# Kernel optimization log

Hardware: AMD Instinct MI355X
Metric: run time of the kernel (lower is better)

Reference implementation:

```python
import jax, jax.numpy as jnp
import numpy as np

N, E, D, H, G = 50000, 800000, 128, 128, 64
EPS = 1e-5


def setup_inputs() -> dict:
    key = jax.random.key(0)
    ks = jax.random.split(key, 16)
    x = jax.random.normal(ks[0], (N, D), dtype=jnp.float32)
    edge_index = jax.random.randint(ks[1], (2, E), 0, N, dtype=jnp.int64)
    batch = jnp.sort(jax.random.randint(ks[2], (N,), 0, G, dtype=jnp.int64))
    dims = [D, H, H, H]
    params = {}
    for i in range(3):
        params[f"W{i}"] = jax.random.normal(ks[3 + i], (dims[i], dims[i + 1]), dtype=jnp.float32) * (1.0 / np.sqrt(dims[i]).astype(np.float32))
        params[f"b{i}"] = jnp.zeros((dims[i + 1],), jnp.float32)
        params[f"g{i}"] = jnp.ones((dims[i + 1],), jnp.float32)   # BN gamma
        params[f"be{i}"] = jnp.zeros((dims[i + 1],), jnp.float32)  # BN beta
    params["Wout"] = jax.random.normal(ks[10], (H, 1), dtype=jnp.float32) * (1.0 / np.sqrt(H).astype(np.float32))
    params["bout"] = jnp.zeros((1,), jnp.float32)
    return {"x": x, "edge_index": edge_index, "batch": batch, **params}


def _gcn_forward(x, edge_index, batch, Ws, bs, gs, bes, Wout, bout):
    n = x.shape[0]
    loop = jnp.arange(n)
    # GCNConv default: add self-loops, symmetric degree normalization
    src = jnp.concatenate([edge_index[0], loop])
    dst = jnp.concatenate([edge_index[1], loop])
    deg = jax.ops.segment_sum(jnp.ones_like(dst, x.dtype), dst, num_segments=n)
    dinv = jax.lax.rsqrt(jnp.maximum(deg, 1.0))  # deg >= 1 from self-loops
    norm = dinv[src] * dinv[dst]                 # [E+N]
    h = x
    for W, b, g, be in zip(Ws, bs, gs, bes):
        h = h @ W                                               # transform [N,C]
        msg = h[src] * norm[:, None]                            # gather [E+N,C]
        h = jax.ops.segment_sum(msg, dst, num_segments=n) + b   # scatter-add
        # BatchNorm1d (training-mode batch statistics over nodes)
        mu = jnp.mean(h, axis=0)
        var = jnp.var(h, axis=0)
        h = (h - mu) * jax.lax.rsqrt(var + EPS) * g + be
        h = jax.nn.relu(h)
        # dropout: identity (deterministic eval reference)
    counts = jax.ops.segment_sum(jnp.ones((n,), h.dtype), batch, num_segments=G)
    pooled = jax.ops.segment_sum(h, batch, num_segments=G) / jnp.maximum(counts, 1.0)[:, None]
    return jax.nn.sigmoid(pooled @ Wout + bout)  # [G,1]


def reference(x, edge_index, batch, W0, b0, g0, be0, W1, b1, g1, be1, W2, b2, g2, be2, Wout, bout):
    return _gcn_forward(x, edge_index, batch,
                        (W0, W1, W2), (b0, b1, b2), (g0, g1, g2), (be0, be1, be2),
                        Wout, bout)
```

## Files before the change

### kernel.cpp

```cpp
#include <hip/hip_runtime.h>

#define EPSBN 1e-5f

using bf16x8 = __attribute__((ext_vector_type(8))) short;
using f32x4  = __attribute__((ext_vector_type(4))) float;

__device__ __forceinline__ unsigned short f2bf(float f) {
    unsigned u = __builtin_bit_cast(unsigned, f);
    unsigned r = (u + 0x7FFFu + ((u >> 16) & 1u)) >> 16;
    return (unsigned short)r;
}
__device__ __forceinline__ float bf2f(unsigned short s) {
    unsigned u = ((unsigned)s) << 16;
    return __builtin_bit_cast(float, u);
}


__global__ void k_deg(const int* __restrict__ dst, int E, int* __restrict__ deg) {
    int i = blockIdx.x * blockDim.x + threadIdx.x;
    if (i < E) atomicAdd(&deg[dst[i]], 1);
}

__global__ void k_dinv(const int* __restrict__ deg, int N, float* __restrict__ dinv) {
    int i = blockIdx.x * blockDim.x + threadIdx.x;
    if (i < N) dinv[i] = rsqrtf((float)(deg[i] + 1));
}

__global__ void k_scan1(const int* __restrict__ deg, int N, int* __restrict__ rs, int* __restrict__ blk) {
    __shared__ int sh[256];
    int tid = threadIdx.x;
    int i = blockIdx.x * 256 + tid;
    int v = (i < N) ? deg[i] : 0;
    sh[tid] = v; __syncthreads();
    for (int off = 1; off < 256; off <<= 1) {
        int t = (tid >= off) ? sh[tid - off] : 0;
        __syncthreads();
        sh[tid] += t;
        __syncthreads();
    }
    if (i < N) rs[i] = sh[tid] - v;
    if (tid == 255) blk[blockIdx.x] = sh[255];
}

__global__ void k_scan2(const int* __restrict__ blk, int nb, int* __restrict__ blkoff) {
    __shared__ int sh[1024];
    int tid = threadIdx.x;
    int v = (tid < nb) ? blk[tid] : 0;
    sh[tid] = v; __syncthreads();
    for (int off = 1; off < 1024; off <<= 1) {
        int t = (tid >= off) ? sh[tid - off] : 0;
        __syncthreads();
        sh[tid] += t;
        __syncthreads();
    }
    if (tid < nb) blkoff[tid] = sh[tid] - v;
}

__global__ void k_scan3(int* __restrict__ rs, int N, const int* __restrict__ blkoff) {
    int i = blockIdx.x * blockDim.x + threadIdx.x;
    if (i < N) rs[i] += blkoff[i >> 8];
}

__global__ void k_fill(const int* __restrict__ src, const int* __restrict__ dst, int E,
                       const int* __restrict__ rs, int* __restrict__ cursor, int* __restrict__ col) {
    int i = blockIdx.x * blockDim.x + threadIdx.x;
    if (i < E) {
        int d = dst[i];
        int pos = rs[d] + atomicAdd(&cursor[d], 1);
        col[pos] = src[i];
    }
}


__global__ __launch_bounds__(256) void k_gemm(const unsigned short* __restrict__ Abf,
                                              const float* __restrict__ Af,
                                              const float* __restrict__ W,
                                              unsigned short* __restrict__ C, int N,
                                              const float* __restrict__ scale,
                                              const float* __restrict__ shift, int mode) {
    __shared__ unsigned short Asw[128 * 128];
    __shared__ unsigned short Wt[128 * 128];
    int tid = threadIdx.x;
    int r0 = blockIdx.x * 128;

    {
        int n = tid & 127, kh = tid >> 7;
        const float* wp = &W[(kh * 64) * 128 + n];
        #pragma unroll
        for (int kb = 0; kb < 8; ++kb) {
            unsigned short t8[8];
            #pragma unroll
            for (int e = 0; e < 8; ++e)
                t8[e] = f2bf(wp[(kb * 8 + e) * 128]);
            int byte = (n * 256 + kh * 128 + kb * 16) ^ ((n & 7) << 4);
            *reinterpret_cast<uint4*>(reinterpret_cast<char*>(Wt) + byte) =
                *reinterpret_cast<const uint4*>(t8);
        }
    }
    if (mode == 0) {
        const float* ap = &Af[(size_t)r0 * 128];
        #pragma unroll
        for (int j = 0; j < 8; ++j) {
            int u = tid + j * 256;
            int row = u >> 4, cg = u & 15;
            unsigned short t8[8] = {0,0,0,0,0,0,0,0};
            if (r0 + row < N) {
                float4 a0 = *reinterpret_cast<const float4*>(ap + row * 128 + cg * 8);
                float4 a1 = *reinterpret_cast<const float4*>(ap + row * 128 + cg * 8 + 4);
                t8[0]=f2bf(a0.x); t8[1]=f2bf(a0.y); t8[2]=f2bf(a0.z); t8[3]=f2bf(a0.w);
                t8[4]=f2bf(a1.x); t8[5]=f2bf(a1.y); t8[6]=f2bf(a1.z); t8[7]=f2bf(a1.w);
            }
            int byte = (row * 256 + cg * 16) ^ ((row & 7) << 4);
            *reinterpret_cast<uint4*>(reinterpret_cast<char*>(Asw) + byte) =
                *reinterpret_cast<const uint4*>(t8);
        }
    } else {
        const unsigned short* ap = &Abf[(size_t)r0 * 128];
        #pragma unroll
        for (int j = 0; j < 8; ++j) {
            int u = tid + j * 256;
            int row = u >> 4, cg = u & 15;
            unsigned short t8[8] = {0,0,0,0,0,0,0,0};
            if (r0 + row < N) {
                ushort4 v0 = *reinterpret_cast<const ushort4*>(ap + (size_t)row * 128 + cg * 8);
                ushort4 v1 = *reinterpret_cast<const ushort4*>(ap + (size_t)row * 128 + cg * 8 + 4);
                float4 sc0 = *reinterpret_cast<const float4*>(&scale[cg * 8]);
                float4 sc1 = *reinterpret_cast<const float4*>(&scale[cg * 8 + 4]);
                float4 sf0 = *reinterpret_cast<const float4*>(&shift[cg * 8]);
                float4 sf1 = *reinterpret_cast<const float4*>(&shift[cg * 8 + 4]);
                t8[0] = f2bf(fmaxf(bf2f(v0.x) * sc0.x + sf0.x, 0.f));
                t8[1] = f2bf(fmaxf(bf2f(v0.y) * sc0.y + sf0.y, 0.f));
                t8[2] = f2bf(fmaxf(bf2f(v0.z) * sc0.z + sf0.z, 0.f));
                t8[3] = f2bf(fmaxf(bf2f(v0.w) * sc0.w + sf0.w, 0.f));
                t8[4] = f2bf(fmaxf(bf2f(v1.x) * sc1.x + sf1.x, 0.f));
                t8[5] = f2bf(fmaxf(bf2f(v1.y) * sc1.y + sf1.y, 0.f));
                t8[6] = f2bf(fmaxf(bf2f(v1.z) * sc1.z + sf1.z, 0.f));
                t8[7] = f2bf(fmaxf(bf2f(v1.w) * sc1.w + sf1.w, 0.f));
            }
            int byte = (row * 256 + cg * 16) ^ ((row & 7) << 4);
            *reinterpret_cast<uint4*>(reinterpret_cast<char*>(Asw) + byte) =
                *reinterpret_cast<const uint4*>(t8);
        }
    }
    __syncthreads();

    int wv = tid >> 6, lane = tid & 63;
    int lr = lane & 15, lk = lane >> 4;
    f32x4 acc[2][8] = {};
    #pragma unroll
    for (int kk = 0; kk < 4; ++kk) {
        bf16x8 af[2], bf[8];
        #pragma unroll
        for (int mf = 0; mf < 2; ++mf) {
            int ar = wv * 32 + mf * 16 + lr;
            int byte = (ar * 256 + kk * 64 + lk * 16) ^ ((ar & 7) << 4);
            af[mf] = *reinterpret_cast<const bf16x8*>(reinterpret_cast<const char*>(Asw) + byte);
        }
        #pragma unroll
        for (int nf = 0; nf < 8; ++nf) {
            int bn = nf * 16 + lr;
            int byte = (bn * 256 + kk * 64 + lk * 16) ^ ((bn & 7) << 4);
            bf[nf] = *reinterpret_cast<const bf16x8*>(reinterpret_cast<const char*>(Wt) + byte);
        }
        #pragma unroll
        for (int mf = 0; mf < 2; ++mf)
            #pragma unroll
            for (int nf = 0; nf < 8; ++nf)
                acc[mf][nf] = __builtin_amdgcn_mfma_f32_16x16x32_bf16(af[mf], bf[nf], acc[mf][nf], 0, 0, 0);
    }
    __syncthreads();
    #pragma unroll
    for (int mf = 0; mf < 2; ++mf)
        #pragma unroll
        for (int nf = 0; nf < 8; ++nf)
            #pragma unroll
            for (int r = 0; r < 4; ++r) {
                int row = wv * 32 + mf * 16 + lk * 4 + r;
                int colc = nf * 16 + lr;
                Asw[row * 128 + colc] = f2bf(acc[mf][nf][r]);
            }
    __syncthreads();
    #pragma unroll
    for (int j = 0; j < 8; ++j) {
        int u = tid + j * 256;
        int row = u >> 4, cg = u & 15;
        if (r0 + row < N)
            *reinterpret_cast<uint4*>(&C[((size_t)(r0 + row)) * 128 + cg * 8]) =
                *reinterpret_cast<const uint4*>(&Asw[row * 128 + cg * 8]);
    }
}


__global__ __launch_bounds__(256) void k_agg(const unsigned short* __restrict__ t, const int* __restrict__ col,
                                             const int* __restrict__ rs, const int* __restrict__ deg,
                                             const float* __restrict__ dinv, const float* __restrict__ bias,
                                             unsigned short* __restrict__ out, int N) {
    int w = (blockIdx.x << 2) + (threadIdx.x >> 6);
    int lane = threadIdx.x & 63;
    if (w >= N) return;
    int start = rs[w], cnt = deg[w];
    float di = dinv[w];
    const ushort2* tp = reinterpret_cast<const ushort2*>(t);
    float ax = 0.f, ay = 0.f;
    int e = 0;
    for (; e + 4 <= cnt; e += 4) {
        int s0 = col[start + e], s1 = col[start + e + 1];
        int s2 = col[start + e + 2], s3 = col[start + e + 3];
        float w0 = dinv[s0], w1 = dinv[s1], w2 = dinv[s2], w3 = dinv[s3];
        ushort2 v0 = tp[(size_t)s0 * 64 + lane];
        ushort2 v1 = tp[(size_t)s1 * 64 + lane];
        ushort2 v2 = tp[(size_t)s2 * 64 + lane];
        ushort2 v3 = tp[(size_t)s3 * 64 + lane];
        ax += w0 * bf2f(v0.x) + w1 * bf2f(v1.x) + w2 * bf2f(v2.x) + w3 * bf2f(v3.x);
        ay += w0 * bf2f(v0.y) + w1 * bf2f(v1.y) + w2 * bf2f(v2.y) + w3 * bf2f(v3.y);
    }
    for (; e < cnt; ++e) {
        int s = col[start + e];
        float ww = dinv[s];
        ushort2 v = tp[(size_t)s * 64 + lane];
        ax += ww * bf2f(v.x);
        ay += ww * bf2f(v.y);
    }
    ushort2 self = tp[(size_t)w * 64 + lane];
    ushort2 o;
    o.x = f2bf(di * ax + di * di * bf2f(self.x) + bias[2 * lane]);
    o.y = f2bf(di * ay + di * di * bf2f(self.y) + bias[2 * lane + 1]);
    reinterpret_cast<ushort2*>(out)[(size_t)w * 64 + lane] = o;
}


__global__ __launch_bounds__(256) void k_stats1(const unsigned short* __restrict__ h, int N,
                                                float* __restrict__ p1, float* __restrict__ p2) {
    int tid = threadIdx.x;
    int cp = tid & 63, rw = tid >> 6;
    float s1x = 0.f, s1y = 0.f, s2x = 0.f, s2y = 0.f;
    const ushort2* hp = reinterpret_cast<const ushort2*>(h);
    for (int i = blockIdx.x * 4 + rw; i < N; i += gridDim.x * 4) {
        ushort2 v = hp[(size_t)i * 64 + cp];
        float x = bf2f(v.x), y = bf2f(v.y);
        s1x += x; s1y += y; s2x += x * x; s2y += y * y;
    }
    __shared__ float sh[4][64][4];
    sh[rw][cp][0] = s1x; sh[rw][cp][1] = s1y; sh[rw][cp][2] = s2x; sh[rw][cp][3] = s2y;
    __syncthreads();
    if (tid < 64) {
        float a0 = 0.f, a1 = 0.f, a2 = 0.f, a3 = 0.f;
        #pragma unroll
        for (int r = 0; r < 4; ++r) {
            a0 += sh[r][tid][0]; a1 += sh[r][tid][1];
            a2 += sh[r][tid][2]; a3 += sh[r][tid][3];
        }
        p1[blockIdx.x * 128 + 2 * tid]     = a0;
        p1[blockIdx.x * 128 + 2 * tid + 1] = a1;
        p2[blockIdx.x * 128 + 2 * tid]     = a2;
        p2[blockIdx.x * 128 + 2 * tid + 1] = a3;
    }
}

__global__ __launch_bounds__(1024) void k_stats2(const float* __restrict__ p1, const float* __restrict__ p2,
                                                 int nb, int N,
                                                 const float* __restrict__ g, const float* __restrict__ be,
                                                 float* __restrict__ scale, float* __restrict__ shift) {
    __shared__ double sh1[1024], sh2[1024];
    int tid = threadIdx.x;
    int c = tid & 127, seg = tid >> 7;
    double s1 = 0.0, s2 = 0.0;
    int b = seg;
    for (; b + 32 <= nb; b += 32) {
        double a0 = p1[(b      ) * 128 + c], q0 = p2[(b      ) * 128 + c];
        double a1 = p1[(b +  8) * 128 + c], q1 = p2[(b +  8) * 128 + c];
        double a2 = p1[(b + 16) * 128 + c], q2 = p2[(b + 16) * 128 + c];
        double a3 = p1[(b + 24) * 128 + c], q3 = p2[(b + 24) * 128 + c];
        s1 += (a0 + a1) + (a2 + a3);
        s2 += (q0 + q1) + (q2 + q3);
    }
    for (; b < nb; b += 8) { s1 += p1[b * 128 + c]; s2 += p2[b * 128 + c]; }
    sh1[tid] = s1; sh2[tid] = s2;
    __syncthreads();
    #pragma unroll
    for (int s = 4; s >= 1; s >>= 1) {
        if (seg < s) {
            sh1[tid] += sh1[tid + s * 128];
            sh2[tid] += sh2[tid + s * 128];
        }
        __syncthreads();
    }
    if (tid < 128) {
        double mu = sh1[c] / N;
        double var = sh2[c] / N - mu * mu;
        double inv = 1.0 / sqrt(var + (double)EPSBN);
        scale[c] = (float)((double)g[c] * inv);
        shift[c] = (float)((double)be[c] - mu * (double)g[c] * inv);
    }
}


__global__ __launch_bounds__(256) void k_pool(const unsigned short* __restrict__ h, const int* __restrict__ batch,
                                              const float* __restrict__ scale, const float* __restrict__ shift,
                                              const float* __restrict__ Wout, int N, int G,
                                              float* __restrict__ pool, int* __restrict__ cnt) {
    __shared__ float pl[64];
    __shared__ int cl[64];
    int tid = threadIdx.x;
    if (tid < 64) { pl[tid] = 0.f; cl[tid] = 0; }
    __syncthreads();
    int wv = tid >> 6, lane = tid & 63;
    float sc0 = scale[2 * lane], sc1 = scale[2 * lane + 1];
    float sf0 = shift[2 * lane], sf1 = shift[2 * lane + 1];
    float w0 = Wout[2 * lane], w1 = Wout[2 * lane + 1];
    const ushort2* hp = reinterpret_cast<const ushort2*>(h);
    int wid = blockIdx.x * 4 + wv;
    int stride = gridDim.x * 4;
    for (int i = wid; i < N; i += stride * 4) {
        int i1 = i + stride, i2 = i + 2 * stride, i3 = i + 3 * stride;
        float s0 = 0.f, s1 = 0.f, s2 = 0.f, s3 = 0.f;
        {
            ushort2 v = hp[(size_t)i * 64 + lane];
            s0 = fmaxf(bf2f(v.x) * sc0 + sf0, 0.f) * w0 + fmaxf(bf2f(v.y) * sc1 + sf1, 0.f) * w1;
        }
        if (i1 < N) {
            ushort2 v = hp[(size_t)i1 * 64 + lane];
            s1 = fmaxf(bf2f(v.x) * sc0 + sf0, 0.f) * w0 + fmaxf(bf2f(v.y) * sc1 + sf1, 0.f) * w1;
        }
        if (i2 < N) {
            ushort2 v = hp[(size_t)i2 * 64 + lane];
            s2 = fmaxf(bf2f(v.x) * sc0 + sf0, 0.f) * w0 + fmaxf(bf2f(v.y) * sc1 + sf1, 0.f) * w1;
        }
        if (i3 < N) {
            ushort2 v = hp[(size_t)i3 * 64 + lane];
            s3 = fmaxf(bf2f(v.x) * sc0 + sf0, 0.f) * w0 + fmaxf(bf2f(v.y) * sc1 + sf1, 0.f) * w1;
        }
        #pragma unroll
        for (int o = 32; o > 0; o >>= 1) {
            s0 += __shfl_down(s0, o); s1 += __shfl_down(s1, o);
            s2 += __shfl_down(s2, o); s3 += __shfl_down(s3, o);
        }
        if (lane == 0) {
            atomicAdd(&pl[batch[i]], s0); atomicAdd(&cl[batch[i]], 1);
            if (i1 < N) { atomicAdd(&pl[batch[i1]], s1); atomicAdd(&cl[batch[i1]], 1); }
            if (i2 < N) { atomicAdd(&pl[batch[i2]], s2); atomicAdd(&cl[batch[i2]], 1); }
            if (i3 < N) { atomicAdd(&pl[batch[i3]], s3); atomicAdd(&cl[batch[i3]], 1); }
        }
    }
    __syncthreads();
    if (tid < 64) {
        atomicAdd(&pool[tid], pl[tid]);
        atomicAdd(&cnt[tid], cl[tid]);
    }
}

__global__ void k_final(const float* __restrict__ pool, const int* __restrict__ cnt,
                        const float* __restrict__ bout, int G, float* __restrict__ out) {
    int g = blockIdx.x * blockDim.x + threadIdx.x;
    if (g < G) {
        float c = fmaxf((float)cnt[g], 1.f);
        float p = pool[g] / c + bout[0];
        out[g] = 1.f / (1.f + expf(-p));
    }
}


extern "C" void kernel_launch(void* const* d_in, const int* in_sizes, int n_in,
                              void* d_out, int out_size, void* d_ws, size_t ws_size,
                              hipStream_t stream) {
    const float* x    = (const float*)d_in[0];
    const int*   ei   = (const int*)d_in[1];
    const int*   batch= (const int*)d_in[2];
    const float* W0p  = (const float*)d_in[3];
    const float* b0p  = (const float*)d_in[4];
    const float* g0p  = (const float*)d_in[5];
    const float* be0p = (const float*)d_in[6];
    const float* W1p  = (const float*)d_in[7];
    const float* b1p  = (const float*)d_in[8];
    const float* g1p  = (const float*)d_in[9];
    const float* be1p = (const float*)d_in[10];
    const float* W2p  = (const float*)d_in[11];
    const float* b2p  = (const float*)d_in[12];
    const float* g2p  = (const float*)d_in[13];
    const float* be2p = (const float*)d_in[14];
    const float* Woutp= (const float*)d_in[15];
    const float* boutp= (const float*)d_in[16];

    int N = in_sizes[0] / 128;
    int E = in_sizes[1] / 2;
    int G = out_size;
    const int* src = ei;
    const int* dst = ei + E;

    char* p = (char*)d_ws;
    auto alloc = [&](size_t bytes) {
        void* q = (void*)p;
        p += (bytes + 255) & ~(size_t)255;
        return q;
    };
    unsigned short* Bt  = (unsigned short*)alloc((size_t)N * 128 * 2);
    unsigned short* Bh  = (unsigned short*)alloc((size_t)N * 128 * 2);
    int*    col    = (int*)   alloc((size_t)E * 4);
    int*    rsA    = (int*)   alloc((size_t)N * 4);
    int*    deg    = (int*)   alloc((size_t)N * 4);
    int*    cursor = (int*)   alloc((size_t)N * 4);
    float*  dinv   = (float*) alloc((size_t)N * 4);
    int*    blk    = (int*)   alloc(1024 * 4);
    int*    blkoff = (int*)   alloc(1024 * 4);
    float*  p1     = (float*) alloc(256 * 128 * 4);
    float*  p2     = (float*) alloc(256 * 128 * 4);
    float*  scale  = (float*) alloc(128 * 4);
    float*  shift  = (float*) alloc(128 * 4);
    float*  pool   = (float*) alloc(64 * 4);
    int*    cnt    = (int*)   alloc(64 * 4);

    hipMemsetAsync(deg, 0, (size_t)N * 4, stream);
    hipMemsetAsync(cursor, 0, (size_t)N * 4, stream);
    hipMemsetAsync(pool, 0, 64 * 4, stream);
    hipMemsetAsync(cnt, 0, 64 * 4, stream);

    int nb = (N + 255) / 256;
    k_deg  <<<(E + 255) / 256, 256, 0, stream>>>(dst, E, deg);
    k_dinv <<<nb, 256, 0, stream>>>(deg, N, dinv);
    k_scan1<<<nb, 256, 0, stream>>>(deg, N, rsA, blk);
    k_scan2<<<1, 1024, 0, stream>>>(blk, nb, blkoff);
    k_scan3<<<nb, 256, 0, stream>>>(rsA, N, blkoff);
    k_fill <<<(E + 255) / 256, 256, 0, stream>>>(src, dst, E, rsA, cursor, col);

    int gemmBlocks = (N + 127) / 128;
    int aggBlocks  = (N + 3) / 4;

    k_gemm  <<<gemmBlocks, 256, 0, stream>>>(nullptr, x, W0p, Bt, N, scale, shift, 0);
    k_agg   <<<aggBlocks, 256, 0, stream>>>(Bt, col, rsA, deg, dinv, b0p, Bh, N);
    k_stats1<<<256, 256, 0, stream>>>(Bh, N, p1, p2);
    k_stats2<<<1, 1024, 0, stream>>>(p1, p2, 256, N, g0p, be0p, scale, shift);
    k_gemm  <<<gemmBlocks, 256, 0, stream>>>(Bh, nullptr, W1p, Bt, N, scale, shift, 1);
    k_agg   <<<aggBlocks, 256, 0, stream>>>(Bt, col, rsA, deg, dinv, b1p, Bh, N);
    k_stats1<<<256, 256, 0, stream>>>(Bh, N, p1, p2);
    k_stats2<<<1, 1024, 0, stream>>>(p1, p2, 256, N, g1p, be1p, scale, shift);
    k_gemm  <<<gemmBlocks, 256, 0, stream>>>(Bh, nullptr, W2p, Bt, N, scale, shift, 1);
    k_agg   <<<aggBlocks, 256, 0, stream>>>(Bt, col, rsA, deg, dinv, b2p, Bh, N);
    k_stats1<<<256, 256, 0, stream>>>(Bh, N, p1, p2);
    k_stats2<<<1, 1024, 0, stream>>>(p1, p2, 256, N, g2p, be2p, scale, shift);
    k_pool <<<256, 256, 0, stream>>>(Bh, batch, scale, shift, Woutp, N, G, pool, cnt);
    k_final<<<1, 64, 0, stream>>>(pool, cnt, boutp, G, (float*)d_out);
}
```

Before: 342.6 us.

## Fuse BN statistics into aggregation and bucket edges before CSR fill

```diff
diff --git a/kernel.cpp b/kernel.cpp
--- a/kernel.cpp
+++ b/kernel.cpp
@@ -1,6 +1,7 @@
 #include <hip/hip_runtime.h>
 
 #define EPSBN 1e-5f
+#define AGG_BLOCKS 2048
 
 using bf16x8 = __attribute__((ext_vector_type(8))) short;
 using f32x4  = __attribute__((ext_vector_type(4))) float;
@@ -16,9 +17,19 @@
 }
 
 
-__global__ void k_deg(const int* __restrict__ dst, int E, int* __restrict__ deg) {
-    int i = blockIdx.x * blockDim.x + threadIdx.x;
-    if (i < E) atomicAdd(&deg[dst[i]], 1);
+__global__ __launch_bounds__(256) void k_bhist(const int* __restrict__ dst, int E,
+                                               int* __restrict__ deg, int* __restrict__ bcnt, int shift) {
+    __shared__ int lh[512];
+    for (int i = threadIdx.x; i < 512; i += 256) lh[i] = 0;
+    __syncthreads();
+    for (int i = blockIdx.x * blockDim.x + threadIdx.x; i < E; i += gridDim.x * blockDim.x) {
+        int d = dst[i];
+        atomicAdd(&deg[d], 1);
+        atomicAdd(&lh[d >> shift], 1);
+    }
+    __syncthreads();
+    for (int i = threadIdx.x; i < 512; i += 256)
+        if (lh[i]) atomicAdd(&bcnt[i], lh[i]);
 }
 
 __global__ void k_dinv(const int* __restrict__ deg, int N, float* __restrict__ dinv) {
@@ -61,13 +72,58 @@
     if (i < N) rs[i] += blkoff[i >> 8];
 }
 
-__global__ void k_fill(const int* __restrict__ src, const int* __restrict__ dst, int E,
-                       const int* __restrict__ rs, int* __restrict__ cursor, int* __restrict__ col) {
-    int i = blockIdx.x * blockDim.x + threadIdx.x;
-    if (i < E) {
-        int d = dst[i];
-        int pos = rs[d] + atomicAdd(&cursor[d], 1);
-        col[pos] = src[i];
+
+__global__ __launch_bounds__(256) void k_bscatter(const int* __restrict__ src, const int* __restrict__ dst, int E,
+                                                  const int* __restrict__ boff, int* __restrict__ gcur,
+                                                  uint2* __restrict__ ebuf, int shift) {
+    __shared__ int lh[512], lb[512];
+    int tid = threadIdx.x;
+    int base = blockIdx.x * 2048;
+    for (int i = tid; i < 512; i += 256) lh[i] = 0;
+    __syncthreads();
+    int ms[8], md[8];
+    #pragma unroll
+    for (int j = 0; j < 8; ++j) {
+        int idx = base + j * 256 + tid;
+        if (idx < E) {
+            ms[j] = src[idx]; md[j] = dst[idx];
+            atomicAdd(&lh[md[j] >> shift], 1);
+        } else md[j] = -1;
+    }
+    __syncthreads();
+    for (int b = tid; b < 512; b += 256) {
+        int c = lh[b];
+        lb[b] = c ? atomicAdd(&gcur[b], c) : 0;
+    }
+    __syncthreads();
+    for (int i = tid; i < 512; i += 256) lh[i] = 0;
+    __syncthreads();
+    #pragma unroll
+    for (int j = 0; j < 8; ++j) {
+        if (md[j] >= 0) {
+            int b = md[j] >> shift;
+            int r = atomicAdd(&lh[b], 1);
+            ebuf[boff[b] + lb[b] + r] = make_uint2((unsigned)ms[j], (unsigned)md[j]);
+        }
+    }
+}
+
+
+__global__ __launch_bounds__(256) void k_fill2(const uint2* __restrict__ ebuf, const int* __restrict__ bcnt,
+                                               const int* __restrict__ boff, const int* __restrict__ rs,
+                                               int* __restrict__ col, int shift) {
+    __shared__ int lcur[256];
+    int b = blockIdx.x;
+    int n0 = b << shift;
+    int cnt = bcnt[b], s = boff[b];
+    int span = 1 << shift;
+    for (int i = threadIdx.x; i < span; i += 256) lcur[i] = 0;
+    __syncthreads();
+    for (int i = threadIdx.x; i < cnt; i += 256) {
+        uint2 e = ebuf[s + i];
+        int d = (int)e.y;
+        int pos = rs[d] + atomicAdd(&lcur[d - n0], 1);
+        col[pos] = (int)e.x;
     }
 }
 
@@ -194,55 +250,47 @@
 __global__ __launch_bounds__(256) void k_agg(const unsigned short* __restrict__ t, const int* __restrict__ col,
                                              const int* __restrict__ rs, const int* __restrict__ deg,
                                              const float* __restrict__ dinv, const float* __restrict__ bias,
-                                             unsigned short* __restrict__ out, int N) {
-    int w = (blockIdx.x << 2) + (threadIdx.x >> 6);
-    int lane = threadIdx.x & 63;
-    if (w >= N) return;
-    int start = rs[w], cnt = deg[w];
-    float di = dinv[w];
+                                             unsigned short* __restrict__ out, int N,
+                                             float* __restrict__ p1, float* __restrict__ p2) {
+    int wv = threadIdx.x >> 6, lane = threadIdx.x & 63;
     const ushort2* tp = reinterpret_cast<const ushort2*>(t);
-    float ax = 0.f, ay = 0.f;
-    int e = 0;
-    for (; e + 4 <= cnt; e += 4) {
-        int s0 = col[start + e], s1 = col[start + e + 1];
-        int s2 = col[start + e + 2], s3 = col[start + e + 3];
-        float w0 = dinv[s0], w1 = dinv[s1], w2 = dinv[s2], w3 = dinv[s3];
-        ushort2 v0 = tp[(size_t)s0 * 64 + lane];
-        ushort2 v1 = tp[(size_t)s1 * 64 + lane];
-        ushort2 v2 = tp[(size_t)s2 * 64 + lane];
-        ushort2 v3 = tp[(size_t)s3 * 64 + lane];
-        ax += w0 * bf2f(v0.x) + w1 * bf2f(v1.x) + w2 * bf2f(v2.x) + w3 * bf2f(v3.x);
-        ay += w0 * bf2f(v0.y) + w1 * bf2f(v1.y) + w2 * bf2f(v2.y) + w3 * bf2f(v3.y);
-    }
-    for (; e < cnt; ++e) {
-        int s = col[start + e];
-        float ww = dinv[s];
-        ushort2 v = tp[(size_t)s * 64 + lane];
-        ax += ww * bf2f(v.x);
-        ay += ww * bf2f(v.y);
-    }
-    ushort2 self = tp[(size_t)w * 64 + lane];
-    ushort2 o;
-    o.x = f2bf(di * ax + di * di * bf2f(self.x) + bias[2 * lane]);
-    o.y = f2bf(di * ay + di * di * bf2f(self.y) + bias[2 * lane + 1]);
-    reinterpret_cast<ushort2*>(out)[(size_t)w * 64 + lane] = o;
-}
-
-
-__global__ __launch_bounds__(256) void k_stats1(const unsigned short* __restrict__ h, int N,
-                                                float* __restrict__ p1, float* __restrict__ p2) {
-    int tid = threadIdx.x;
-    int cp = tid & 63, rw = tid >> 6;
+    float b0 = bias[2 * lane], b1 = bias[2 * lane + 1];
     float s1x = 0.f, s1y = 0.f, s2x = 0.f, s2y = 0.f;
-    const ushort2* hp = reinterpret_cast<const ushort2*>(h);
-    for (int i = blockIdx.x * 4 + rw; i < N; i += gridDim.x * 4) {
-        ushort2 v = hp[(size_t)i * 64 + cp];
-        float x = bf2f(v.x), y = bf2f(v.y);
-        s1x += x; s1y += y; s2x += x * x; s2y += y * y;
+    for (int w = blockIdx.x * 4 + wv; w < N; w += gridDim.x * 4) {
+        int start = rs[w], cnt = deg[w];
+        float di = dinv[w];
+        float ax = 0.f, ay = 0.f;
+        int e = 0;
+        for (; e + 4 <= cnt; e += 4) {
+            int s0 = col[start + e], s1 = col[start + e + 1];
+            int s2 = col[start + e + 2], s3 = col[start + e + 3];
+            float w0 = dinv[s0], w1 = dinv[s1], w2 = dinv[s2], w3 = dinv[s3];
+            ushort2 v0 = tp[(size_t)s0 * 64 + lane];
+            ushort2 v1 = tp[(size_t)s1 * 64 + lane];
+            ushort2 v2 = tp[(size_t)s2 * 64 + lane];
+            ushort2 v3 = tp[(size_t)s3 * 64 + lane];
+            ax += w0 * bf2f(v0.x) + w1 * bf2f(v1.x) + w2 * bf2f(v2.x) + w3 * bf2f(v3.x);
+            ay += w0 * bf2f(v0.y) + w1 * bf2f(v1.y) + w2 * bf2f(v2.y) + w3 * bf2f(v3.y);
+        }
+        for (; e < cnt; ++e) {
+            int s = col[start + e];
+            float ww = dinv[s];
+            ushort2 v = tp[(size_t)s * 64 + lane];
+            ax += ww * bf2f(v.x);
+            ay += ww * bf2f(v.y);
+        }
+        ushort2 self = tp[(size_t)w * 64 + lane];
+        ushort2 o;
+        o.x = f2bf(di * ax + di * di * bf2f(self.x) + b0);
+        o.y = f2bf(di * ay + di * di * bf2f(self.y) + b1);
+        reinterpret_cast<ushort2*>(out)[(size_t)w * 64 + lane] = o;
+        float rx = bf2f(o.x), ry = bf2f(o.y);
+        s1x += rx; s1y += ry; s2x += rx * rx; s2y += ry * ry;
     }
     __shared__ float sh[4][64][4];
-    sh[rw][cp][0] = s1x; sh[rw][cp][1] = s1y; sh[rw][cp][2] = s2x; sh[rw][cp][3] = s2y;
-    __syncthreads();
+    sh[wv][lane][0] = s1x; sh[wv][lane][1] = s1y; sh[wv][lane][2] = s2x; sh[wv][lane][3] = s2y;
+    __syncthreads();
+    int tid = threadIdx.x;
     if (tid < 64) {
         float a0 = 0.f, a1 = 0.f, a2 = 0.f, a3 = 0.f;
         #pragma unroll
@@ -255,6 +303,21 @@
         p2[blockIdx.x * 128 + 2 * tid]     = a2;
         p2[blockIdx.x * 128 + 2 * tid + 1] = a3;
     }
+}
+
+
+__global__ __launch_bounds__(128) void k_statsmid(const float* __restrict__ p1, const float* __restrict__ p2,
+                                                  int rows, float* __restrict__ pm1, float* __restrict__ pm2) {
+    int c = threadIdx.x, b = blockIdx.x;
+    int r0 = b * rows;
+    float s1 = 0.f, s2 = 0.f;
+    #pragma unroll 4
+    for (int r = 0; r < rows; ++r) {
+        s1 += p1[(size_t)(r0 + r) * 128 + c];
+        s2 += p2[(size_t)(r0 + r) * 128 + c];
+    }
+    pm1[b * 128 + c] = s1;
+    pm2[b * 128 + c] = s2;
 }
 
 __global__ __launch_bounds__(1024) void k_stats2(const float* __restrict__ p1, const float* __restrict__ p2,
@@ -387,6 +450,10 @@
     const int* src = ei;
     const int* dst = ei + E;
 
+    int shiftB = 7;
+    while ((((N + (1 << shiftB) - 1) >> shiftB) > 512) && shiftB < 8) ++shiftB;
+    int nbuck = (N + (1 << shiftB) - 1) >> shiftB;
+
     char* p = (char*)d_ws;
     auto alloc = [&](size_t bytes) {
         void* q = (void*)p;
@@ -396,47 +463,55 @@
     unsigned short* Bt  = (unsigned short*)alloc((size_t)N * 128 * 2);
     unsigned short* Bh  = (unsigned short*)alloc((size_t)N * 128 * 2);
     int*    col    = (int*)   alloc((size_t)E * 4);
+    uint2*  ebuf   = (uint2*) alloc((size_t)E * 8);
     int*    rsA    = (int*)   alloc((size_t)N * 4);
     int*    deg    = (int*)   alloc((size_t)N * 4);
-    int*    cursor = (int*)   alloc((size_t)N * 4);
     float*  dinv   = (float*) alloc((size_t)N * 4);
     int*    blk    = (int*)   alloc(1024 * 4);
     int*    blkoff = (int*)   alloc(1024 * 4);
-    float*  p1     = (float*) alloc(256 * 128 * 4);
-    float*  p2     = (float*) alloc(256 * 128 * 4);
+    int*    bcnt   = (int*)   alloc(512 * 4);
+    int*    boff   = (int*)   alloc(512 * 4);
+    int*    gcur   = (int*)   alloc(512 * 4);
+    float*  p1     = (float*) alloc((size_t)AGG_BLOCKS * 128 * 4);
+    float*  p2     = (float*) alloc((size_t)AGG_BLOCKS * 128 * 4);
+    float*  pm1    = (float*) alloc(128 * 128 * 4);
+    float*  pm2    = (float*) alloc(128 * 128 * 4);
     float*  scale  = (float*) alloc(128 * 4);
     float*  shift  = (float*) alloc(128 * 4);
     float*  pool   = (float*) alloc(64 * 4);
     int*    cnt    = (int*)   alloc(64 * 4);
 
     hipMemsetAsync(deg, 0, (size_t)N * 4, stream);
-    hipMemsetAsync(cursor, 0, (size_t)N * 4, stream);
+    hipMemsetAsync(bcnt, 0, 512 * 4, stream);
+    hipMemsetAsync(gcur, 0, 512 * 4, stream);
     hipMemsetAsync(pool, 0, 64 * 4, stream);
     hipMemsetAsync(cnt, 0, 64 * 4, stream);
 
     int nb = (N + 255) / 256;
-    k_deg  <<<(E + 255) / 256, 256, 0, stream>>>(dst, E, deg);
-    k_dinv <<<nb, 256, 0, stream>>>(deg, N, dinv);
-    k_scan1<<<nb, 256, 0, stream>>>(deg, N, rsA, blk);
-    k_scan2<<<1, 1024, 0, stream>>>(blk, nb, blkoff);
-    k_scan3<<<nb, 256, 0, stream>>>(rsA, N, blkoff);
-    k_fill <<<(E + 255) / 256, 256, 0, stream>>>(src, dst, E, rsA, cursor, col);
+    k_bhist   <<<256, 256, 0, stream>>>(dst, E, deg, bcnt, shiftB);
+    k_dinv    <<<nb, 256, 0, stream>>>(deg, N, dinv);
+    k_scan1   <<<nb, 256, 0, stream>>>(deg, N, rsA, blk);
+    k_scan2   <<<1, 1024, 0, stream>>>(blk, nb, blkoff);
+    k_scan3   <<<nb, 256, 0, stream>>>(rsA, N, blkoff);
+    k_scan2   <<<1, 1024, 0, stream>>>(bcnt, 512, boff);
+    k_bscatter<<<(E + 2047) / 2048, 256, 0, stream>>>(src, dst, E, boff, gcur, ebuf, shiftB);
+    k_fill2   <<<nbuck, 256, 0, stream>>>(ebuf, bcnt, boff, rsA, col, shiftB);
 
     int gemmBlocks = (N + 127) / 128;
-    int aggBlocks  = (N + 3) / 4;
-
-    k_gemm  <<<gemmBlocks, 256, 0, stream>>>(nullptr, x, W0p, Bt, N, scale, shift, 0);
-    k_agg   <<<aggBlocks, 256, 0, stream>>>(Bt, col, rsA, deg, dinv, b0p, Bh, N);
-    k_stats1<<<256, 256, 0, stream>>>(Bh, N, p1, p2);
-    k_stats2<<<1, 1024, 0, stream>>>(p1, p2, 256, N, g0p, be0p, scale, shift);
-    k_gemm  <<<gemmBlocks, 256, 0, stream>>>(Bh, nullptr, W1p, Bt, N, scale, shift, 1);
-    k_agg   <<<aggBlocks, 256, 0, stream>>>(Bt, col, rsA, deg, dinv, b1p, Bh, N);
-    k_stats1<<<256, 256, 0, stream>>>(Bh, N, p1, p2);
-    k_stats2<<<1, 1024, 0, stream>>>(p1, p2, 256, N, g1p, be1p, scale, shift);
-    k_gemm  <<<gemmBlocks, 256, 0, stream>>>(Bh, nullptr, W2p, Bt, N, scale, shift, 1);
-    k_agg   <<<aggBlocks, 256, 0, stream>>>(Bt, col, rsA, deg, dinv, b2p, Bh, N);
-    k_stats1<<<256, 256, 0, stream>>>(Bh, N, p1, p2);
-    k_stats2<<<1, 1024, 0, stream>>>(p1, p2, 256, N, g2p, be2p, scale, shift);
+    int midRows = AGG_BLOCKS / 128;
+
+    k_gemm    <<<gemmBlocks, 256, 0, stream>>>(nullptr, x, W0p, Bt, N, scale, shift, 0);
+    k_agg     <<<AGG_BLOCKS, 256, 0, stream>>>(Bt, col, rsA, deg, dinv, b0p, Bh, N, p1, p2);
+    k_statsmid<<<128, 128, 0, stream>>>(p1, p2, midRows, pm1, pm2);
+    k_stats2  <<<1, 1024, 0, stream>>>(pm1, pm2, 128, N, g0p, be0p, scale, shift);
+    k_gemm    <<<gemmBlocks, 256, 0, stream>>>(Bh, nullptr, W1p, Bt, N, scale, shift, 1);
+    k_agg     <<<AGG_BLOCKS, 256, 0, stream>>>(Bt, col, rsA, deg, dinv, b1p, Bh, N, p1, p2);
+    k_statsmid<<<128, 128, 0, stream>>>(p1, p2, midRows, pm1, pm2);
+    k_stats2  <<<1, 1024, 0, stream>>>(pm1, pm2, 128, N, g1p, be1p, scale, shift);
+    k_gemm    <<<gemmBlocks, 256, 0, stream>>>(Bh, nullptr, W2p, Bt, N, scale, shift, 1);
+    k_agg     <<<AGG_BLOCKS, 256, 0, stream>>>(Bt, col, rsA, deg, dinv, b2p, Bh, N, p1, p2);
+    k_statsmid<<<128, 128, 0, stream>>>(p1, p2, midRows, pm1, pm2);
+    k_stats2  <<<1, 1024, 0, stream>>>(pm1, pm2, 128, N, g2p, be2p, scale, shift);
     k_pool <<<256, 256, 0, stream>>>(Bh, batch, scale, shift, Woutp, N, G, pool, cnt);
     k_final<<<1, 64, 0, stream>>>(pool, cnt, boutp, G, (float*)d_out);
 }
```

New measurement: 300.6 us. -12.3%, faster.
